# Performance work log

Measured on AMD Instinct MI355X. Metric: run time of the kernel, lower is better.

The kernel has to match this reference:

```python
import jax, jax.numpy as jnp
import numpy as np
import math

WH, WW = 7, 7          # window size
N = WH * WW            # tokens per window = 49
H = 12                 # num heads
C = 384                # dim
D = C // H             # head dim = 32
NW = 64                # num windows (56x56 map, 7x7 windows)
B = 32                 # image batch
BW = B * NW            # windowed batch = 2048


def _cpb_constants():
    # log-spaced continuous relative coords table, flattened to [(2*WH-1)*(2*WW-1), 2]
    rh = np.arange(-(WH - 1), WH, dtype=np.float32)
    rw = np.arange(-(WW - 1), WW, dtype=np.float32)
    t = np.stack(np.meshgrid(rh, rw, indexing='ij'), axis=-1)  # [13,13,2]
    t[..., 0] /= (WH - 1)
    t[..., 1] /= (WW - 1)
    t *= 8.0
    t = np.sign(t) * np.log2(np.abs(t) + 1.0) / np.log2(8.0)
    # relative position index [N*N]
    ch, cw = np.meshgrid(np.arange(WH), np.arange(WW), indexing='ij')
    cf = np.stack([ch.ravel(), cw.ravel()])            # [2, N]
    rel = cf[:, :, None] - cf[:, None, :]              # [2, N, N]
    rel = rel.transpose(1, 2, 0).astype(np.int64)      # [N, N, 2]
    rel[..., 0] += WH - 1
    rel[..., 1] += WW - 1
    rel[..., 0] *= 2 * WW - 1
    rpi = rel.sum(-1).reshape(-1)                      # [N*N]
    return jnp.asarray(t.reshape(-1, 2)), jnp.asarray(rpi)

_COORDS_TABLE, _RPI = _cpb_constants()


def setup_inputs() -> dict:
    key = jax.random.key(0)
    ks = jax.random.split(key, 8)
    x = jax.random.normal(ks[0], (BW, N, C), dtype=jnp.float32)
    # shifted-window style 0/-100 mask
    mask = jnp.where(jax.random.uniform(ks[1], (NW, N, N)) < 0.1, -100.0, 0.0).astype(jnp.float32)
    qkv_w = jax.random.normal(ks[2], (3 * C, C), dtype=jnp.float32) * 0.02
    q_bias = jnp.zeros((C,), dtype=jnp.float32)
    v_bias = jnp.zeros((C,), dtype=jnp.float32)
    logit_scale = jnp.full((H, 1, 1), math.log(10.0), dtype=jnp.float32)
    cpb_w1 = jax.random.normal(ks[3], (512, 2), dtype=jnp.float32) * 0.02
    cpb_b1 = jnp.zeros((512,), dtype=jnp.float32)
    cpb_w2 = jax.random.normal(ks[4], (H, 512), dtype=jnp.float32) * 0.02
    proj_w = jax.random.normal(ks[5], (C, C), dtype=jnp.float32) * 0.02
    proj_b = jnp.zeros((C,), dtype=jnp.float32)
    return {"x": x, "mask": mask, "qkv_w": qkv_w, "q_bias": q_bias, "v_bias": v_bias,
            "logit_scale": logit_scale, "cpb_w1": cpb_w1, "cpb_b1": cpb_b1,
            "cpb_w2": cpb_w2, "proj_w": proj_w, "proj_b": proj_b}


def reference(x, mask, qkv_w, q_bias, v_bias, logit_scale, cpb_w1, cpb_b1, cpb_w2, proj_w, proj_b):
    B_, n, c = x.shape
    # qkv projection; k has no bias (registered zeros buffer)
    qkv_bias = jnp.concatenate([q_bias, jnp.zeros_like(q_bias), v_bias])
    qkv = x @ qkv_w.T + qkv_bias                              # [B_, N, 3C]
    qkv = qkv.reshape(B_, n, 3, H, D).transpose(2, 0, 3, 1, 4)  # [3, B_, H, N, D]
    q, k, v = qkv[0], qkv[1], qkv[2]
    # cosine attention
    qn = q / jnp.clip(jnp.linalg.norm(q, axis=-1, keepdims=True), 1e-12)
    kn = k / jnp.clip(jnp.linalg.norm(k, axis=-1, keepdims=True), 1e-12)
    attn = jnp.einsum('bhnd,bhmd->bhnm', qn, kn)              # [B_, H, N, N]
    scale = jnp.exp(jnp.minimum(logit_scale, math.log(1.0 / 0.01)))  # [H,1,1]
    attn = attn * scale
    # continuous position bias MLP + gather
    hid = jax.nn.relu(_COORDS_TABLE @ cpb_w1.T + cpb_b1)      # [169, 512]
    bias_tab = hid @ cpb_w2.T                                  # [169, H]
    rpb = bias_tab[_RPI].reshape(n, n, H).transpose(2, 0, 1)  # [H, N, N]
    rpb = 16.0 * jax.nn.sigmoid(rpb)
    attn = attn + rpb[None]
    # shifted-window mask add
    nW = mask.shape[0]
    attn = attn.reshape(B_ // nW, nW, H, n, n) + mask[None, :, None]
    attn = jax.nn.softmax(attn.reshape(B_, H, n, n), axis=-1)
    out = jnp.einsum('bhnm,bhmd->bnhd', attn, v).reshape(B_, n, c)
    return out @ proj_w.T + proj_b
```

## Files before the change

### kernel.cpp

```cpp
#include <hip/hip_runtime.h>
#include <hip/hip_bf16.h>
#include <math.h>

#define NTOK 49
#define NH 12
#define HD 32
#define CDIM 384
#define NWIN 64
#define BWIN 2048
#define QKVROW 1152

typedef __bf16 bf16x8 __attribute__((ext_vector_type(8)));
typedef __bf16 bf16x4 __attribute__((ext_vector_type(4)));
typedef float f32x4 __attribute__((ext_vector_type(4)));

__device__ __forceinline__ void gload_lds16(const void* g, void* l) {
    __builtin_amdgcn_global_load_lds((const __attribute__((address_space(1))) void*)g,
                                     (__attribute__((address_space(3))) void*)l, 16, 0, 0);
}

__device__ __forceinline__ void cvt8(const float* src, __bf16* dst, int i) {
    f32x4 a = *(const f32x4*)(src + (size_t)i * 8);
    f32x4 b = *(const f32x4*)(src + (size_t)i * 8 + 4);
    bf16x8 o;
#pragma unroll
    for (int e = 0; e < 4; ++e) { o[e] = (__bf16)a[e]; o[e + 4] = (__bf16)b[e]; }
    *(bf16x8*)(dst + (size_t)i * 8) = o;
}

#define XBLKS 18816
__global__ void prep1(const float* __restrict__ x, __bf16* __restrict__ xbf,
                      const float* __restrict__ qkv_w, __bf16* __restrict__ qkv_wb,
                      const float* __restrict__ proj_w, __bf16* __restrict__ proj_wb,
                      const float* __restrict__ w1, const float* __restrict__ b1,
                      const float* __restrict__ w2, float* __restrict__ bias_tab) {
    const int blk = blockIdx.x, tid = threadIdx.x;
    if (blk < XBLKS) {
        cvt8(x, xbf, blk * 256 + tid);
    } else if (blk < XBLKS + 216) {
        cvt8(qkv_w, qkv_wb, (blk - XBLKS) * 256 + tid);
    } else if (blk < XBLKS + 288) {
        cvt8(proj_w, proj_wb, (blk - XBLKS - 216) * 256 + tid);
    } else {
        int t = (blk - XBLKS - 288) * 256 + tid;
        if (t >= 169 * NH) return;
        int r = t / NH, h = t - (t / NH) * NH;
        int i = r / 13, j = r - (r / 13) * 13;
        float a0 = (float)(i - 6) * (8.0f / 6.0f);
        float a1 = (float)(j - 6) * (8.0f / 6.0f);
        float c0 = copysignf(log2f(fabsf(a0) + 1.0f) * (1.0f / 3.0f), a0);
        float c1 = copysignf(log2f(fabsf(a1) + 1.0f) * (1.0f / 3.0f), a1);
        float sum = 0.f;
        for (int k = 0; k < 512; ++k) {
            float hid = c0 * w1[2 * k] + c1 * w1[2 * k + 1] + b1[k];
            hid = fmaxf(hid, 0.f);
            sum += hid * w2[h * 512 + k];
        }
        bias_tab[r * NH + h] = sum;
    }
}

__global__ void prep2(const float* __restrict__ bias_tab, const float* __restrict__ mask,
                      float* __restrict__ biasC) {
    int idx = blockIdx.x * blockDim.x + threadIdx.x;
    if (idx >= NWIN * NH * NTOK * NTOK) return;
    const int per_w = NH * NTOK * NTOK;
    int w = idx / per_w;
    int rem = idx - w * per_w;
    int h = rem / (NTOK * NTOK);
    int kq = rem - h * (NTOK * NTOK);
    int k = kq / NTOK, q = kq - (kq / NTOK) * NTOK;
    int chi = q / 7, cwi = q - chi * 7;
    int chj = k / 7, cwj = k - chj * 7;
    int rpi = (chi - chj + 6) * 13 + (cwi - cwj + 6);
    float r = bias_tab[rpi * NH + h];
    biasC[idx] = 16.f / (1.f + __expf(-r)) + mask[(w * NTOK + q) * NTOK + k];
}

template <int MODE, int NBY>
__global__ __launch_bounds__(256) void gemm6(
    const __bf16* __restrict__ A, const __bf16* __restrict__ Bw,
    const float* __restrict__ qbias, const float* __restrict__ vbias,
    __bf16* __restrict__ qkvout,
    float* __restrict__ fout, const float* __restrict__ fbias)
{
    __shared__ __bf16 As[3][128 * 32];
    __shared__ __bf16 Bs[3][128 * 32];
    const int tid = threadIdx.x;
    const int chunk = (784 * NBY) >> 3;
    const int wg = (blockIdx.x & 7) * chunk + (blockIdx.x >> 3);
    const int gx = wg / NBY, gy = wg - (wg / NBY) * NBY;
    const int lane = tid & 63;
    const int wid = tid >> 6;
    const int wr = (wid >> 1) * 64;
    const int wc = (wid & 1) * 64;
    const int fr = lane & 15;
    const int fq = lane >> 4;

    f32x4 acc[4][4];
#pragma unroll
    for (int m = 0; m < 4; ++m)
#pragma unroll
        for (int n = 0; n < 4; ++n)
            acc[m][n] = (f32x4){0.f, 0.f, 0.f, 0.f};

    const int srow0 = tid >> 2, scp0 = tid & 3;
    const int srow1 = (256 + tid) >> 2;
    const size_t ar0 = (size_t)(gx * 128 + srow0) * CDIM + (scp0 ^ ((srow0 >> 1) & 3)) * 8;
    const size_t ar1 = (size_t)(gx * 128 + srow1) * CDIM + (scp0 ^ ((srow1 >> 1) & 3)) * 8;
    const size_t br0 = (size_t)(gy * 128 + srow0) * CDIM + (scp0 ^ ((srow0 >> 1) & 3)) * 8;
    const size_t br1 = (size_t)(gy * 128 + srow1) * CDIM + (scp0 ^ ((srow1 >> 1) & 3)) * 8;
    const int ls0 = tid * 16, ls1 = (256 + tid) * 16;

#define STAGE(ti, buf) do {                                              \
        const int kk_ = (ti) * 32;                                       \
        gload_lds16(A + ar0 + kk_, (char*)&As[buf][0] + ls0);            \
        gload_lds16(A + ar1 + kk_, (char*)&As[buf][0] + ls1);            \
        gload_lds16(Bw + br0 + kk_, (char*)&Bs[buf][0] + ls0);           \
        gload_lds16(Bw + br1 + kk_, (char*)&Bs[buf][0] + ls1);           \
    } while (0)

    STAGE(0, 0);
    STAGE(1, 1);

#pragma unroll
    for (int t = 0; t < 12; ++t) {
        if (t < 11) asm volatile("s_waitcnt vmcnt(4)" ::: "memory");
        else        asm volatile("s_waitcnt vmcnt(0)" ::: "memory");
        __builtin_amdgcn_s_barrier();
        if (t + 2 < 12) STAGE(t + 2, (t + 2) % 3);
        const int cur = t % 3;
        bf16x8 af[4], bfr[4];
#pragma unroll
        for (int m = 0; m < 4; ++m) {
            const int row = wr + m * 16 + fr;
            af[m] = *(const bf16x8*)&As[cur][row * 32 + (fq ^ ((row >> 1) & 3)) * 8];
        }
#pragma unroll
        for (int n = 0; n < 4; ++n) {
            const int row = wc + n * 16 + fr;
            bfr[n] = *(const bf16x8*)&Bs[cur][row * 32 + (fq ^ ((row >> 1) & 3)) * 8];
        }
#pragma unroll
        for (int m = 0; m < 4; ++m)
#pragma unroll
            for (int n = 0; n < 4; ++n)
                acc[m][n] = __builtin_amdgcn_mfma_f32_16x16x32_bf16(af[m], bfr[n], acc[m][n], 0, 0, 0);
    }
#undef STAGE

    if (MODE == 0) {
        const int colbase = gy * 128;
        const int part = colbase / CDIM;
        const int pcolbase = colbase - part * CDIM;
#pragma unroll
        for (int m = 0; m < 4; ++m) {
#pragma unroll
            for (int r = 0; r < 4; ++r) {
                const int row = gx * 128 + wr + m * 16 + fq * 4 + r;
                __bf16* orow = qkvout + (size_t)row * QKVROW + colbase + wc;
#pragma unroll
                for (int n = 0; n < 4; ++n) {
                    const int pcol = pcolbase + wc + n * 16 + fr;
                    float val = acc[m][n][r];
                    if (part == 0) val += qbias[pcol];
                    if (part == 2) val += vbias[pcol];
                    orow[n * 16 + fr] = (__bf16)val;
                }
            }
        }
    } else {
#pragma unroll
        for (int m = 0; m < 4; ++m) {
#pragma unroll
            for (int r = 0; r < 4; ++r) {
                const int row = gx * 128 + wr + m * 16 + fq * 4 + r;
                float* orow = fout + (size_t)row * CDIM + gy * 128 + wc;
#pragma unroll
                for (int n = 0; n < 4; ++n) {
                    const int col = gy * 128 + wc + n * 16 + fr;
                    orow[n * 16 + fr] = acc[m][n][r] + fbias[col];
                }
            }
        }
    }
}

#define WREG 15872
__global__ __launch_bounds__(256) void attn2(
    const __bf16* __restrict__ qkv, const float* __restrict__ biasC,
    const float* __restrict__ lscale, __bf16* __restrict__ aout)
{
    __shared__ char smem[4 * WREG];
    const int tid = threadIdx.x;
    const int wid = tid >> 6, lane = tid & 63;
    const int bh = blockIdx.x * 4 + wid;
    const int b = bh / NH, h = bh - b * NH;
    const int w = b & (NWIN - 1);
    const int c = lane & 15, g = lane >> 4;

    char* base = smem + wid * WREG;
    __bf16* Kl = (__bf16*)base;
    __bf16* Ql = (__bf16*)(base + 5120);
    __bf16* Vl = (__bf16*)(base + 10240);
    float* invq = (float*)(base + 15360);
    float* invk = (float*)(base + 15616);
    char* Pl = base;

    const float sc = __expf(fminf(lscale[h], 4.6051702f));

    {
        const int row = lane;
        const size_t rb = ((size_t)b * NTOK + row) * QKVROW + h * HD;
        bf16x8 z;
#pragma unroll
        for (int e = 0; e < 8; ++e) z[e] = (__bf16)0.f;
        {
            bf16x8 t[4];
            float ss = 0.f;
            if (row < NTOK) {
#pragma unroll
                for (int ch = 0; ch < 4; ++ch) {
                    t[ch] = *(const bf16x8*)(qkv + rb + ch * 8);
#pragma unroll
                    for (int e = 0; e < 8; ++e) { float f = (float)t[ch][e]; ss += f * f; }
                }
            } else {
#pragma unroll
                for (int ch = 0; ch < 4; ++ch) t[ch] = z;
            }
#pragma unroll
            for (int ch = 0; ch < 4; ++ch) *(bf16x8*)&Ql[row * 40 + ch * 8] = t[ch];
            invq[row] = sc / fmaxf(sqrtf(ss), 1e-12f);
        }
        {
            bf16x8 t[4];
            float ss = 0.f;
            if (row < NTOK) {
#pragma unroll
                for (int ch = 0; ch < 4; ++ch) {
                    t[ch] = *(const bf16x8*)(qkv + rb + CDIM + ch * 8);
#pragma unroll
                    for (int e = 0; e < 8; ++e) { float f = (float)t[ch][e]; ss += f * f; }
                }
            } else {
#pragma unroll
                for (int ch = 0; ch < 4; ++ch) t[ch] = z;
            }
#pragma unroll
            for (int ch = 0; ch < 4; ++ch) *(bf16x8*)&Kl[row * 40 + ch * 8] = t[ch];
            invk[row] = 1.f / fmaxf(sqrtf(ss), 1e-12f);
        }
        {
            bf16x8 t[4];
            if (row < NTOK) {
#pragma unroll
                for (int ch = 0; ch < 4; ++ch) t[ch] = *(const bf16x8*)(qkv + rb + 2 * CDIM + ch * 8);
            } else {
#pragma unroll
                for (int ch = 0; ch < 4; ++ch) t[ch] = z;
            }
#pragma unroll
            for (int ch = 0; ch < 4; ++ch) *(bf16x8*)&Vl[row * 40 + ch * 8] = t[ch];
        }
    }

    bf16x8 kfr[4], qfr[4];
#pragma unroll
    for (int mt = 0; mt < 4; ++mt) kfr[mt] = *(const bf16x8*)&Kl[(mt * 16 + c) * 40 + g * 8];
#pragma unroll
    for (int nt = 0; nt < 4; ++nt) qfr[nt] = *(const bf16x8*)&Ql[(nt * 16 + c) * 40 + g * 8];
    f32x4 S[4][4];
#pragma unroll
    for (int mt = 0; mt < 4; ++mt)
#pragma unroll
        for (int nt = 0; nt < 4; ++nt) {
            S[mt][nt] = (f32x4){0.f, 0.f, 0.f, 0.f};
            S[mt][nt] = __builtin_amdgcn_mfma_f32_16x16x32_bf16(kfr[mt], qfr[nt], S[mt][nt], 0, 0, 0);
        }

    const float* bc = biasC + ((size_t)(w * NH + h)) * (NTOK * NTOK);
    float ivq[4];
#pragma unroll
    for (int nt = 0; nt < 4; ++nt) ivq[nt] = invq[nt * 16 + c];
#pragma unroll
    for (int mt = 0; mt < 4; ++mt) {
#pragma unroll
        for (int r = 0; r < 4; ++r) {
            const int k = mt * 16 + g * 4 + r;
            const float ivk = invk[k];
#pragma unroll
            for (int nt = 0; nt < 4; ++nt) {
                const int q = nt * 16 + c;
                float v = S[mt][nt][r] * ivk * ivq[nt];
                if (k < NTOK) {
                    if (q < NTOK) v += bc[k * NTOK + q];
                } else {
                    v = -1e30f;
                }
                S[mt][nt][r] = v;
            }
        }
    }

    float rs[4];
#pragma unroll
    for (int nt = 0; nt < 4; ++nt) {
        float m = -1e30f;
#pragma unroll
        for (int mt = 0; mt < 4; ++mt)
#pragma unroll
            for (int r = 0; r < 4; ++r) m = fmaxf(m, S[mt][nt][r]);
        m = fmaxf(m, __shfl_xor(m, 16));
        m = fmaxf(m, __shfl_xor(m, 32));
        float s = 0.f;
#pragma unroll
        for (int mt = 0; mt < 4; ++mt)
#pragma unroll
            for (int r = 0; r < 4; ++r) {
                float e = __expf(S[mt][nt][r] - m);
                S[mt][nt][r] = e;
                s += e;
            }
        s += __shfl_xor(s, 16);
        s += __shfl_xor(s, 32);
        rs[nt] = 1.f / s;
    }

#pragma unroll
    for (int mt = 0; mt < 4; ++mt)
#pragma unroll
        for (int nt = 0; nt < 4; ++nt) {
            bf16x4 pk;
#pragma unroll
            for (int r = 0; r < 4; ++r) pk[r] = (__bf16)(S[mt][nt][r] * rs[nt]);
            *(bf16x4*)(Pl + (nt * 16 + c) * 144 + (mt * 16 + g * 4) * 2) = pk;
        }

    bf16x8 vfr[2][2];
#pragma unroll
    for (int kt = 0; kt < 2; ++kt)
#pragma unroll
        for (int dt = 0; dt < 2; ++dt) {
            bf16x8 t;
#pragma unroll
            for (int e = 0; e < 8; ++e) t[e] = Vl[(kt * 32 + g * 8 + e) * 40 + dt * 16 + c];
            vfr[kt][dt] = t;
        }
    f32x4 O[4][2];
#pragma unroll
    for (int mt = 0; mt < 4; ++mt)
#pragma unroll
        for (int dt = 0; dt < 2; ++dt) O[mt][dt] = (f32x4){0.f, 0.f, 0.f, 0.f};
#pragma unroll
    for (int mt = 0; mt < 4; ++mt)
#pragma unroll
        for (int kt = 0; kt < 2; ++kt) {
            bf16x8 pfr = *(const bf16x8*)(Pl + (mt * 16 + c) * 144 + kt * 64 + g * 16);
#pragma unroll
            for (int dt = 0; dt < 2; ++dt)
                O[mt][dt] = __builtin_amdgcn_mfma_f32_16x16x32_bf16(pfr, vfr[kt][dt], O[mt][dt], 0, 0, 0);
        }

#pragma unroll
    for (int mt = 0; mt < 4; ++mt)
#pragma unroll
        for (int r = 0; r < 4; ++r) {
            const int q = mt * 16 + g * 4 + r;
            if (q < NTOK) {
                const size_t off = ((size_t)b * NTOK + q) * CDIM + h * HD;
                aout[off + c] = (__bf16)O[mt][0][r];
                aout[off + 16 + c] = (__bf16)O[mt][1][r];
            }
        }
}

extern "C" void kernel_launch(void* const* d_in, const int* in_sizes, int n_in,
                              void* d_out, int out_size, void* d_ws, size_t ws_size,
                              hipStream_t stream) {
    const float* x      = (const float*)d_in[0];
    const float* mask   = (const float*)d_in[1];
    const float* qkv_w  = (const float*)d_in[2];
    const float* q_bias = (const float*)d_in[3];
    const float* v_bias = (const float*)d_in[4];
    const float* lscale = (const float*)d_in[5];
    const float* cpb_w1 = (const float*)d_in[6];
    const float* cpb_b1 = (const float*)d_in[7];
    const float* cpb_w2 = (const float*)d_in[8];
    const float* proj_w = (const float*)d_in[9];
    const float* proj_b = (const float*)d_in[10];
    float* out = (float*)d_out;

    const size_t NROWS = (size_t)BWIN * NTOK;
    __bf16* qkvbuf  = (__bf16*)d_ws;
    __bf16* xbf     = qkvbuf + NROWS * QKVROW;
    __bf16* aoutbuf = xbf;
    __bf16* qkv_wb  = xbf + NROWS * CDIM;
    __bf16* proj_wb = qkv_wb + QKVROW * CDIM;
    float*  bias_tab = (float*)(proj_wb + CDIM * CDIM);
    float*  biasC   = bias_tab + 169 * NH;

    hipLaunchKernelGGL(prep1, dim3(XBLKS + 296), dim3(256), 0, stream,
                       x, xbf, qkv_w, qkv_wb, proj_w, proj_wb,
                       cpb_w1, cpb_b1, cpb_w2, bias_tab);
    hipLaunchKernelGGL(prep2, dim3((NWIN * NH * NTOK * NTOK + 255) / 256), dim3(256), 0, stream,
                       bias_tab, mask, biasC);
    hipLaunchKernelGGL((gemm6<0, 9>), dim3(784 * 9), dim3(256), 0, stream,
                       xbf, qkv_wb, q_bias, v_bias, qkvbuf, (float*)nullptr,
                       (const float*)nullptr);
    hipLaunchKernelGGL(attn2, dim3(BWIN * NH / 4), dim3(256), 0, stream,
                       qkvbuf, biasC, lscale, aoutbuf);
    hipLaunchKernelGGL((gemm6<1, 3>), dim3(784 * 3), dim3(256), 0, stream,
                       aoutbuf, proj_wb, (const float*)nullptr, (const float*)nullptr,
                       (__bf16*)nullptr, out, proj_b);
}
```

Before: 448.3 us.

## Reorganize attention blocks per window-head with LDS-cached bias and prefetched QKV

The attention kernel now assigns each block one (window, head) pair and half of the batch. The block stages the combined position/mask bias once in LDS and reuses it across 16 images, and each wave loops over 4 images while prefetching the next image's Q/K/V into registers. MFMA sections are wrapped in s_setprio. This cuts repeated global bias reads and hides load latency, at the cost of fewer blocks (1536 instead of 6144), more LDS and more register pressure. Missing barriers between loop iterations within a wave are probably safe, since each wave owns its own LDS region and executes in lockstep.

```diff
diff --git a/kernel.cpp b/kernel.cpp
--- a/kernel.cpp
+++ b/kernel.cpp
@@ -187,17 +187,25 @@
 }
 
 #define WREG 15872
-__global__ __launch_bounds__(256) void attn2(
+__global__ __launch_bounds__(256) void attn4(
     const __bf16* __restrict__ qkv, const float* __restrict__ biasC,
     const float* __restrict__ lscale, __bf16* __restrict__ aout)
 {
-    __shared__ char smem[4 * WREG];
+    __shared__ char smem[4 * WREG + 9604];
+    float* bcs = (float*)(smem + 4 * WREG);
     const int tid = threadIdx.x;
     const int wid = tid >> 6, lane = tid & 63;
-    const int bh = blockIdx.x * 4 + wid;
-    const int b = bh / NH, h = bh - b * NH;
-    const int w = b & (NWIN - 1);
+    const int blk = blockIdx.x;
+    const int wh = blk >> 1, half = blk & 1;
+    const int w = wh / NH, h = wh - (wh / NH) * NH;
     const int c = lane & 15, g = lane >> 4;
+    const int row = lane;
+
+    {
+        const float* src = biasC + (size_t)(w * NH + h) * (NTOK * NTOK);
+        for (int i = tid; i < NTOK * NTOK; i += 256) bcs[i] = src[i];
+    }
+    __syncthreads();
 
     char* base = smem + wid * WREG;
     __bf16* Kl = (__bf16*)base;
@@ -209,170 +217,180 @@
 
     const float sc = __expf(fminf(lscale[h], 4.6051702f));
 
+    bf16x8 z;
+#pragma unroll
+    for (int e = 0; e < 8; ++e) z[e] = (__bf16)0.f;
+
+    bf16x8 qc[4], kc[4], vc[4];
     {
-        const int row = lane;
-        const size_t rb = ((size_t)b * NTOK + row) * QKVROW + h * HD;
-        bf16x8 z;
-#pragma unroll
-        for (int e = 0; e < 8; ++e) z[e] = (__bf16)0.f;
+        const int b0 = (half * 16 + wid * 4) * NWIN + w;
+        const size_t rb = ((size_t)b0 * NTOK + row) * QKVROW + h * HD;
+        if (row < NTOK) {
+#pragma unroll
+            for (int ch = 0; ch < 4; ++ch) {
+                qc[ch] = *(const bf16x8*)(qkv + rb + ch * 8);
+                kc[ch] = *(const bf16x8*)(qkv + rb + CDIM + ch * 8);
+                vc[ch] = *(const bf16x8*)(qkv + rb + 2 * CDIM + ch * 8);
+            }
+        } else {
+#pragma unroll
+            for (int ch = 0; ch < 4; ++ch) { qc[ch] = z; kc[ch] = z; vc[ch] = z; }
+        }
+    }
+
+    for (int img = 0; img < 4; ++img) {
+        const int b = (half * 16 + wid * 4 + img) * NWIN + w;
+
+        bf16x8 qn[4], kn[4], vn[4];
+        if (img < 3) {
+            const size_t rb2 = ((size_t)(b + NWIN) * NTOK + row) * QKVROW + h * HD;
+            if (row < NTOK) {
+#pragma unroll
+                for (int ch = 0; ch < 4; ++ch) {
+                    qn[ch] = *(const bf16x8*)(qkv + rb2 + ch * 8);
+                    kn[ch] = *(const bf16x8*)(qkv + rb2 + CDIM + ch * 8);
+                    vn[ch] = *(const bf16x8*)(qkv + rb2 + 2 * CDIM + ch * 8);
+                }
+            } else {
+#pragma unroll
+                for (int ch = 0; ch < 4; ++ch) { qn[ch] = z; kn[ch] = z; vn[ch] = z; }
+            }
+        }
+
         {
-            bf16x8 t[4];
-            float ss = 0.f;
-            if (row < NTOK) {
-#pragma unroll
-                for (int ch = 0; ch < 4; ++ch) {
-                    t[ch] = *(const bf16x8*)(qkv + rb + ch * 8);
-#pragma unroll
-                    for (int e = 0; e < 8; ++e) { float f = (float)t[ch][e]; ss += f * f; }
-                }
-            } else {
-#pragma unroll
-                for (int ch = 0; ch < 4; ++ch) t[ch] = z;
-            }
-#pragma unroll
-            for (int ch = 0; ch < 4; ++ch) *(bf16x8*)&Ql[row * 40 + ch * 8] = t[ch];
-            invq[row] = sc / fmaxf(sqrtf(ss), 1e-12f);
-        }
-        {
-            bf16x8 t[4];
-            float ss = 0.f;
-            if (row < NTOK) {
-#pragma unroll
-                for (int ch = 0; ch < 4; ++ch) {
-                    t[ch] = *(const bf16x8*)(qkv + rb + CDIM + ch * 8);
-#pragma unroll
-                    for (int e = 0; e < 8; ++e) { float f = (float)t[ch][e]; ss += f * f; }
-                }
-            } else {
-#pragma unroll
-                for (int ch = 0; ch < 4; ++ch) t[ch] = z;
-            }
-#pragma unroll
-            for (int ch = 0; ch < 4; ++ch) *(bf16x8*)&Kl[row * 40 + ch * 8] = t[ch];
-            invk[row] = 1.f / fmaxf(sqrtf(ss), 1e-12f);
-        }
-        {
-            bf16x8 t[4];
-            if (row < NTOK) {
-#pragma unroll
-                for (int ch = 0; ch < 4; ++ch) t[ch] = *(const bf16x8*)(qkv + rb + 2 * CDIM + ch * 8);
-            } else {
-#pragma unroll
-                for (int ch = 0; ch < 4; ++ch) t[ch] = z;
-            }
-#pragma unroll
-            for (int ch = 0; ch < 4; ++ch) *(bf16x8*)&Vl[row * 40 + ch * 8] = t[ch];
-        }
-    }
-
-    bf16x8 kfr[4], qfr[4];
-#pragma unroll
-    for (int mt = 0; mt < 4; ++mt) kfr[mt] = *(const bf16x8*)&Kl[(mt * 16 + c) * 40 + g * 8];
-#pragma unroll
-    for (int nt = 0; nt < 4; ++nt) qfr[nt] = *(const bf16x8*)&Ql[(nt * 16 + c) * 40 + g * 8];
-    f32x4 S[4][4];
-#pragma unroll
-    for (int mt = 0; mt < 4; ++mt)
+            float ssq = 0.f, ssk = 0.f;
+#pragma unroll
+            for (int ch = 0; ch < 4; ++ch) {
+                *(bf16x8*)&Ql[row * 40 + ch * 8] = qc[ch];
+                *(bf16x8*)&Kl[row * 40 + ch * 8] = kc[ch];
+                *(bf16x8*)&Vl[row * 40 + ch * 8] = vc[ch];
+#pragma unroll
+                for (int e = 0; e < 8; ++e) {
+                    float fq_ = (float)qc[ch][e]; ssq += fq_ * fq_;
+                    float fk_ = (float)kc[ch][e]; ssk += fk_ * fk_;
+                }
+            }
+            invq[row] = sc / fmaxf(sqrtf(ssq), 1e-12f);
+            invk[row] = 1.f / fmaxf(sqrtf(ssk), 1e-12f);
+        }
+
+        bf16x8 kfr[4], qfr[4];
+#pragma unroll
+        for (int mt = 0; mt < 4; ++mt) kfr[mt] = *(const bf16x8*)&Kl[(mt * 16 + c) * 40 + g * 8];
+#pragma unroll
+        for (int nt = 0; nt < 4; ++nt) qfr[nt] = *(const bf16x8*)&Ql[(nt * 16 + c) * 40 + g * 8];
+        f32x4 S[4][4];
+        __builtin_amdgcn_s_setprio(1);
+#pragma unroll
+        for (int mt = 0; mt < 4; ++mt)
+#pragma unroll
+            for (int nt = 0; nt < 4; ++nt) {
+                S[mt][nt] = (f32x4){0.f, 0.f, 0.f, 0.f};
+                S[mt][nt] = __builtin_amdgcn_mfma_f32_16x16x32_bf16(kfr[mt], qfr[nt], S[mt][nt], 0, 0, 0);
+            }
+        __builtin_amdgcn_s_setprio(0);
+
+        float ivq[4];
+#pragma unroll
+        for (int nt = 0; nt < 4; ++nt) ivq[nt] = invq[nt * 16 + c];
+#pragma unroll
+        for (int mt = 0; mt < 4; ++mt) {
+#pragma unroll
+            for (int r = 0; r < 4; ++r) {
+                const int k = mt * 16 + g * 4 + r;
+                const float ivk = invk[k];
+#pragma unroll
+                for (int nt = 0; nt < 4; ++nt) {
+                    const int q = nt * 16 + c;
+                    float v = S[mt][nt][r] * ivk * ivq[nt];
+                    if (k < NTOK) {
+                        if (q < NTOK) v += bcs[k * NTOK + q];
+                    } else {
+                        v = -1e30f;
+                    }
+                    S[mt][nt][r] = v;
+                }
+            }
+        }
+
+        float rs[4];
 #pragma unroll
         for (int nt = 0; nt < 4; ++nt) {
-            S[mt][nt] = (f32x4){0.f, 0.f, 0.f, 0.f};
-            S[mt][nt] = __builtin_amdgcn_mfma_f32_16x16x32_bf16(kfr[mt], qfr[nt], S[mt][nt], 0, 0, 0);
-        }
-
-    const float* bc = biasC + ((size_t)(w * NH + h)) * (NTOK * NTOK);
-    float ivq[4];
-#pragma unroll
-    for (int nt = 0; nt < 4; ++nt) ivq[nt] = invq[nt * 16 + c];
-#pragma unroll
-    for (int mt = 0; mt < 4; ++mt) {
-#pragma unroll
-        for (int r = 0; r < 4; ++r) {
-            const int k = mt * 16 + g * 4 + r;
-            const float ivk = invk[k];
+            float m = -1e30f;
+#pragma unroll
+            for (int mt = 0; mt < 4; ++mt)
+#pragma unroll
+                for (int r = 0; r < 4; ++r) m = fmaxf(m, S[mt][nt][r]);
+            m = fmaxf(m, __shfl_xor(m, 16));
+            m = fmaxf(m, __shfl_xor(m, 32));
+            float s = 0.f;
+#pragma unroll
+            for (int mt = 0; mt < 4; ++mt)
+#pragma unroll
+                for (int r = 0; r < 4; ++r) {
+                    float e = __expf(S[mt][nt][r] - m);
+                    S[mt][nt][r] = e;
+                    s += e;
+                }
+            s += __shfl_xor(s, 16);
+            s += __shfl_xor(s, 32);
+            rs[nt] = 1.f / s;
+        }
+
+#pragma unroll
+        for (int mt = 0; mt < 4; ++mt)
 #pragma unroll
             for (int nt = 0; nt < 4; ++nt) {
-                const int q = nt * 16 + c;
-                float v = S[mt][nt][r] * ivk * ivq[nt];
-                if (k < NTOK) {
-                    if (q < NTOK) v += bc[k * NTOK + q];
-                } else {
-                    v = -1e30f;
-                }
-                S[mt][nt][r] = v;
-            }
-        }
-    }
-
-    float rs[4];
-#pragma unroll
-    for (int nt = 0; nt < 4; ++nt) {
-        float m = -1e30f;
+                bf16x4 pk;
+#pragma unroll
+                for (int r = 0; r < 4; ++r) pk[r] = (__bf16)(S[mt][nt][r] * rs[nt]);
+                *(bf16x4*)(Pl + (nt * 16 + c) * 144 + (mt * 16 + g * 4) * 2) = pk;
+            }
+
+        bf16x8 vfr[2][2];
+#pragma unroll
+        for (int kt = 0; kt < 2; ++kt)
+#pragma unroll
+            for (int dt = 0; dt < 2; ++dt) {
+                bf16x8 t;
+#pragma unroll
+                for (int e = 0; e < 8; ++e) t[e] = Vl[(kt * 32 + g * 8 + e) * 40 + dt * 16 + c];
+                vfr[kt][dt] = t;
+            }
+        f32x4 O[4][2];
 #pragma unroll
         for (int mt = 0; mt < 4; ++mt)
 #pragma unroll
-            for (int r = 0; r < 4; ++r) m = fmaxf(m, S[mt][nt][r]);
-        m = fmaxf(m, __shfl_xor(m, 16));
-        m = fmaxf(m, __shfl_xor(m, 32));
-        float s = 0.f;
+            for (int dt = 0; dt < 2; ++dt) O[mt][dt] = (f32x4){0.f, 0.f, 0.f, 0.f};
+        __builtin_amdgcn_s_setprio(1);
 #pragma unroll
         for (int mt = 0; mt < 4; ++mt)
 #pragma unroll
+            for (int kt = 0; kt < 2; ++kt) {
+                bf16x8 pfr = *(const bf16x8*)(Pl + (mt * 16 + c) * 144 + kt * 64 + g * 16);
+#pragma unroll
+                for (int dt = 0; dt < 2; ++dt)
+                    O[mt][dt] = __builtin_amdgcn_mfma_f32_16x16x32_bf16(pfr, vfr[kt][dt], O[mt][dt], 0, 0, 0);
+            }
+        __builtin_amdgcn_s_setprio(0);
+
+#pragma unroll
+        for (int mt = 0; mt < 4; ++mt)
+#pragma unroll
             for (int r = 0; r < 4; ++r) {
-                float e = __expf(S[mt][nt][r] - m);
-                S[mt][nt][r] = e;
-                s += e;
-            }
-        s += __shfl_xor(s, 16);
-        s += __shfl_xor(s, 32);
-        rs[nt] = 1.f / s;
-    }
-
-#pragma unroll
-    for (int mt = 0; mt < 4; ++mt)
-#pragma unroll
-        for (int nt = 0; nt < 4; ++nt) {
-            bf16x4 pk;
-#pragma unroll
-            for (int r = 0; r < 4; ++r) pk[r] = (__bf16)(S[mt][nt][r] * rs[nt]);
-            *(bf16x4*)(Pl + (nt * 16 + c) * 144 + (mt * 16 + g * 4) * 2) = pk;
-        }
-
-    bf16x8 vfr[2][2];
-#pragma unroll
-    for (int kt = 0; kt < 2; ++kt)
-#pragma unroll
-        for (int dt = 0; dt < 2; ++dt) {
-            bf16x8 t;
-#pragma unroll
-            for (int e = 0; e < 8; ++e) t[e] = Vl[(kt * 32 + g * 8 + e) * 40 + dt * 16 + c];
-            vfr[kt][dt] = t;
-        }
-    f32x4 O[4][2];
-#pragma unroll
-    for (int mt = 0; mt < 4; ++mt)
-#pragma unroll
-        for (int dt = 0; dt < 2; ++dt) O[mt][dt] = (f32x4){0.f, 0.f, 0.f, 0.f};
-#pragma unroll
-    for (int mt = 0; mt < 4; ++mt)
-#pragma unroll
-        for (int kt = 0; kt < 2; ++kt) {
-            bf16x8 pfr = *(const bf16x8*)(Pl + (mt * 16 + c) * 144 + kt * 64 + g * 16);
-#pragma unroll
-            for (int dt = 0; dt < 2; ++dt)
-                O[mt][dt] = __builtin_amdgcn_mfma_f32_16x16x32_bf16(pfr, vfr[kt][dt], O[mt][dt], 0, 0, 0);
-        }
-
-#pragma unroll
-    for (int mt = 0; mt < 4; ++mt)
-#pragma unroll
-        for (int r = 0; r < 4; ++r) {
-            const int q = mt * 16 + g * 4 + r;
-            if (q < NTOK) {
-                const size_t off = ((size_t)b * NTOK + q) * CDIM + h * HD;
-                aout[off + c] = (__bf16)O[mt][0][r];
-                aout[off + 16 + c] = (__bf16)O[mt][1][r];
-            }
-        }
+                const int q = mt * 16 + g * 4 + r;
+                if (q < NTOK) {
+                    const size_t off = ((size_t)b * NTOK + q) * CDIM + h * HD;
+                    aout[off + c] = (__bf16)O[mt][0][r];
+                    aout[off + 16 + c] = (__bf16)O[mt][1][r];
+                }
+            }
+
+        if (img < 3) {
+#pragma unroll
+            for (int ch = 0; ch < 4; ++ch) { qc[ch] = qn[ch]; kc[ch] = kn[ch]; vc[ch] = vn[ch]; }
+        }
+    }
 }
 
 extern "C" void kernel_launch(void* const* d_in, const int* in_sizes, int n_in,
@@ -408,7 +426,7 @@
     hipLaunchKernelGGL((gemm6<0, 9>), dim3(784 * 9), dim3(256), 0, stream,
                        xbf, qkv_wb, q_bias, v_bias, qkvbuf, (float*)nullptr,
                        (const float*)nullptr);
-    hipLaunchKernelGGL(attn2, dim3(BWIN * NH / 4), dim3(256), 0, stream,
+    hipLaunchKernelGGL(attn4, dim3(NWIN * NH * 2), dim3(256), 0, stream,
                        qkvbuf, biasC, lscale, aoutbuf);
     hipLaunchKernelGGL((gemm6<1, 3>), dim3(784 * 3), dim3(256), 0, stream,
                        aoutbuf, proj_wb, (const float*)nullptr, (const float*)nullptr,
```

After: 490.5 us. 9.4% more time.

## Load Q/K fragments directly from global and shrink attention LDS footprint

Applied to the files above, without the earlier changes.

The attention kernel now loads Q and K MFMA fragments straight from global memory into registers and computes row norms with cross-lane shuffles, so Q and K no longer go through LDS. Only V is still staged in LDS. The probability matrix is written and consumed in two 32-key halves, so the P buffer shrinks to an 80-byte row stride and the per-wave LDS region drops from 15872 to 10496 bytes. The aim is fewer LDS round trips and higher occupancy, at the cost of more scattered global loads and extra shuffles.

```diff
diff --git a/kernel.cpp b/kernel.cpp
--- a/kernel.cpp
+++ b/kernel.cpp
@@ -186,12 +186,12 @@
     }
 }
 
-#define WREG 15872
-__global__ __launch_bounds__(256) void attn2(
+#define AWREG 10496
+__global__ __launch_bounds__(256) void attn5(
     const __bf16* __restrict__ qkv, const float* __restrict__ biasC,
     const float* __restrict__ lscale, __bf16* __restrict__ aout)
 {
-    __shared__ char smem[4 * WREG];
+    __shared__ char smem[4 * AWREG];
     const int tid = threadIdx.x;
     const int wid = tid >> 6, lane = tid & 63;
     const int bh = blockIdx.x * 4 + wid;
@@ -199,77 +199,65 @@
     const int w = b & (NWIN - 1);
     const int c = lane & 15, g = lane >> 4;
 
-    char* base = smem + wid * WREG;
-    __bf16* Kl = (__bf16*)base;
-    __bf16* Ql = (__bf16*)(base + 5120);
-    __bf16* Vl = (__bf16*)(base + 10240);
-    float* invq = (float*)(base + 15360);
-    float* invk = (float*)(base + 15616);
-    char* Pl = base;
+    char* base = smem + wid * AWREG;
+    __bf16* Vl = (__bf16*)base;
+    char* Pl = base + 5120;
+    float* invk = (float*)(base + 10240);
 
     const float sc = __expf(fminf(lscale[h], 4.6051702f));
+
+    bf16x8 z;
+#pragma unroll
+    for (int e = 0; e < 8; ++e) z[e] = (__bf16)0.f;
+
+    const size_t wbase = (size_t)b * NTOK * QKVROW + h * HD;
 
     {
         const int row = lane;
-        const size_t rb = ((size_t)b * NTOK + row) * QKVROW + h * HD;
-        bf16x8 z;
-#pragma unroll
-        for (int e = 0; e < 8; ++e) z[e] = (__bf16)0.f;
-        {
-            bf16x8 t[4];
-            float ss = 0.f;
-            if (row < NTOK) {
-#pragma unroll
-                for (int ch = 0; ch < 4; ++ch) {
-                    t[ch] = *(const bf16x8*)(qkv + rb + ch * 8);
-#pragma unroll
-                    for (int e = 0; e < 8; ++e) { float f = (float)t[ch][e]; ss += f * f; }
-                }
-            } else {
-#pragma unroll
-                for (int ch = 0; ch < 4; ++ch) t[ch] = z;
-            }
-#pragma unroll
-            for (int ch = 0; ch < 4; ++ch) *(bf16x8*)&Ql[row * 40 + ch * 8] = t[ch];
-            invq[row] = sc / fmaxf(sqrtf(ss), 1e-12f);
-        }
-        {
-            bf16x8 t[4];
-            float ss = 0.f;
-            if (row < NTOK) {
-#pragma unroll
-                for (int ch = 0; ch < 4; ++ch) {
-                    t[ch] = *(const bf16x8*)(qkv + rb + CDIM + ch * 8);
-#pragma unroll
-                    for (int e = 0; e < 8; ++e) { float f = (float)t[ch][e]; ss += f * f; }
-                }
-            } else {
-#pragma unroll
-                for (int ch = 0; ch < 4; ++ch) t[ch] = z;
-            }
-#pragma unroll
-            for (int ch = 0; ch < 4; ++ch) *(bf16x8*)&Kl[row * 40 + ch * 8] = t[ch];
-            invk[row] = 1.f / fmaxf(sqrtf(ss), 1e-12f);
-        }
-        {
-            bf16x8 t[4];
-            if (row < NTOK) {
-#pragma unroll
-                for (int ch = 0; ch < 4; ++ch) t[ch] = *(const bf16x8*)(qkv + rb + 2 * CDIM + ch * 8);
-            } else {
-#pragma unroll
-                for (int ch = 0; ch < 4; ++ch) t[ch] = z;
-            }
-#pragma unroll
-            for (int ch = 0; ch < 4; ++ch) *(bf16x8*)&Vl[row * 40 + ch * 8] = t[ch];
-        }
-    }
-
-    bf16x8 kfr[4], qfr[4];
-#pragma unroll
-    for (int mt = 0; mt < 4; ++mt) kfr[mt] = *(const bf16x8*)&Kl[(mt * 16 + c) * 40 + g * 8];
-#pragma unroll
-    for (int nt = 0; nt < 4; ++nt) qfr[nt] = *(const bf16x8*)&Ql[(nt * 16 + c) * 40 + g * 8];
+        bf16x8 t[4];
+        if (row < NTOK) {
+            const __bf16* p = qkv + wbase + (size_t)row * QKVROW + 2 * CDIM;
+#pragma unroll
+            for (int ch = 0; ch < 4; ++ch) t[ch] = *(const bf16x8*)(p + ch * 8);
+        } else {
+#pragma unroll
+            for (int ch = 0; ch < 4; ++ch) t[ch] = z;
+        }
+#pragma unroll
+        for (int ch = 0; ch < 4; ++ch) *(bf16x8*)&Vl[row * 40 + ch * 8] = t[ch];
+    }
+
+    bf16x8 kfr[4];
+#pragma unroll
+    for (int mt = 0; mt < 4; ++mt) {
+        const int row = mt * 16 + c;
+        kfr[mt] = (row < NTOK)
+            ? *(const bf16x8*)(qkv + wbase + (size_t)row * QKVROW + CDIM + g * 8)
+            : z;
+        float ss = 0.f;
+#pragma unroll
+        for (int e = 0; e < 8; ++e) { float f = (float)kfr[mt][e]; ss += f * f; }
+        ss += __shfl_xor(ss, 16);
+        ss += __shfl_xor(ss, 32);
+        if (g == 0) invk[row] = 1.f / fmaxf(sqrtf(ss), 1e-12f);
+    }
+
+    bf16x8 qfr[4];
+    float ivq[4];
+#pragma unroll
+    for (int nt = 0; nt < 4; ++nt) {
+        const int row = nt * 16 + c;
+        qfr[nt] = (row < NTOK)
+            ? *(const bf16x8*)(qkv + wbase + (size_t)row * QKVROW + g * 8)
+            : z;
+        float ss = 0.f;
+#pragma unroll
+        for (int e = 0; e < 8; ++e) { float f = (float)qfr[nt][e]; ss += f * f; }
+        ss += __shfl_xor(ss, 16);
+        ss += __shfl_xor(ss, 32);
+        ivq[nt] = sc / fmaxf(sqrtf(ss), 1e-12f);
+    }
+
     f32x4 S[4][4];
 #pragma unroll
     for (int mt = 0; mt < 4; ++mt)
@@ -280,9 +268,6 @@
         }
 
     const float* bc = biasC + ((size_t)(w * NH + h)) * (NTOK * NTOK);
-    float ivq[4];
-#pragma unroll
-    for (int nt = 0; nt < 4; ++nt) ivq[nt] = invq[nt * 16 + c];
 #pragma unroll
     for (int mt = 0; mt < 4; ++mt) {
 #pragma unroll
@@ -327,40 +312,41 @@
         rs[nt] = 1.f / s;
     }
 
+    f32x4 O[4][2];
 #pragma unroll
     for (int mt = 0; mt < 4; ++mt)
 #pragma unroll
-        for (int nt = 0; nt < 4; ++nt) {
-            bf16x4 pk;
-#pragma unroll
-            for (int r = 0; r < 4; ++r) pk[r] = (__bf16)(S[mt][nt][r] * rs[nt]);
-            *(bf16x4*)(Pl + (nt * 16 + c) * 144 + (mt * 16 + g * 4) * 2) = pk;
-        }
-
-    bf16x8 vfr[2][2];
-#pragma unroll
-    for (int kt = 0; kt < 2; ++kt)
+        for (int dt = 0; dt < 2; ++dt) O[mt][dt] = (f32x4){0.f, 0.f, 0.f, 0.f};
+
+#pragma unroll
+    for (int kt = 0; kt < 2; ++kt) {
+#pragma unroll
+        for (int mtl = 0; mtl < 2; ++mtl) {
+            const int mt = kt * 2 + mtl;
+#pragma unroll
+            for (int nt = 0; nt < 4; ++nt) {
+                bf16x4 pk;
+#pragma unroll
+                for (int r = 0; r < 4; ++r) pk[r] = (__bf16)(S[mt][nt][r] * rs[nt]);
+                *(bf16x4*)(Pl + (nt * 16 + c) * 80 + (mtl * 16 + g * 4) * 2) = pk;
+            }
+        }
+        bf16x8 vfr[2];
 #pragma unroll
         for (int dt = 0; dt < 2; ++dt) {
             bf16x8 t;
 #pragma unroll
             for (int e = 0; e < 8; ++e) t[e] = Vl[(kt * 32 + g * 8 + e) * 40 + dt * 16 + c];
-            vfr[kt][dt] = t;
-        }
-    f32x4 O[4][2];
-#pragma unroll
-    for (int mt = 0; mt < 4; ++mt)
-#pragma unroll
-        for (int dt = 0; dt < 2; ++dt) O[mt][dt] = (f32x4){0.f, 0.f, 0.f, 0.f};
-#pragma unroll
-    for (int mt = 0; mt < 4; ++mt)
-#pragma unroll
-        for (int kt = 0; kt < 2; ++kt) {
-            bf16x8 pfr = *(const bf16x8*)(Pl + (mt * 16 + c) * 144 + kt * 64 + g * 16);
+            vfr[dt] = t;
+        }
+#pragma unroll
+        for (int mtO = 0; mtO < 4; ++mtO) {
+            bf16x8 pfr = *(const bf16x8*)(Pl + (mtO * 16 + c) * 80 + g * 16);
 #pragma unroll
             for (int dt = 0; dt < 2; ++dt)
-                O[mt][dt] = __builtin_amdgcn_mfma_f32_16x16x32_bf16(pfr, vfr[kt][dt], O[mt][dt], 0, 0, 0);
-        }
+                O[mtO][dt] = __builtin_amdgcn_mfma_f32_16x16x32_bf16(pfr, vfr[dt], O[mtO][dt], 0, 0, 0);
+        }
+    }
 
 #pragma unroll
     for (int mt = 0; mt < 4; ++mt)
@@ -408,7 +394,7 @@
     hipLaunchKernelGGL((gemm6<0, 9>), dim3(784 * 9), dim3(256), 0, stream,
                        xbf, qkv_wb, q_bias, v_bias, qkvbuf, (float*)nullptr,
                        (const float*)nullptr);
-    hipLaunchKernelGGL(attn2, dim3(BWIN * NH / 4), dim3(256), 0, stream,
+    hipLaunchKernelGGL(attn5, dim3(BWIN * NH / 4), dim3(256), 0, stream,
                        qkvbuf, biasC, lscale, aoutbuf);
     hipLaunchKernelGGL((gemm6<1, 3>), dim3(784 * 3), dim3(256), 0, stream,
                        aoutbuf, proj_wb, (const float*)nullptr, (const float*)nullptr,
```

New measurement: 476.3 us. 6.2% more time.
